# Kernel optimization log

Hardware: AMD Instinct MI355X
Metric: run time of the kernel (lower is better)

## Reference

```python
import jax, jax.numpy as jnp
import numpy as np

HEADS = 16

def rotate_half(x):
    x1, x2 = jnp.split(x, 2, axis=-1)
    return jnp.concatenate((-x2, x1), axis=-1)

def setup_inputs() -> dict:
    key = jax.random.key(0)
    k1, k2, k3, k4 = jax.random.split(key, 4)
    b, n, h = 2, 2048, 1024
    d = h // HEADS
    x = jax.random.normal(k1, (b, n, h), dtype=jnp.float32)
    rotary_emb = jax.random.normal(k2, (n, d), dtype=jnp.float32)
    w_qkv = jax.random.normal(k3, (h, 3 * h), dtype=jnp.float32) * (1.0 / np.sqrt(h))
    w_out = jax.random.normal(k4, (h, h), dtype=jnp.float32) * (1.0 / np.sqrt(h))
    return {"x": x, "rotary_emb": rotary_emb, "w_qkv": w_qkv, "w_out": w_out}

def reference(x, rotary_emb, w_qkv, w_out):
    b, n, hidden = x.shape
    d = hidden // HEADS
    # fused QKV projection: [b,n,3*hidden]
    qkv = jnp.einsum('bnh,hk->bnk', x, w_qkv)
    q, k, v = jnp.split(qkv, 3, axis=-1)
    # [b,n,hidden] -> [b,H,n,d]
    split_heads = lambda t: t.reshape(b, n, HEADS, d).transpose(0, 2, 1, 3)
    q, k, v = split_heads(q), split_heads(k), split_heads(v)
    # rotary: pos is [n,d], broadcast over batch/heads
    cos = jnp.cos(rotary_emb)[None, None]
    sin = jnp.sin(rotary_emb)[None, None]
    q = q * cos + rotate_half(q) * sin
    k = k * cos + rotate_half(k) * sin
    # SDPA (no mask, no dropout)
    scale = 1.0 / np.sqrt(d).astype(np.float32)
    scores = jnp.einsum('bhqd,bhkd->bhqk', q, k) * scale
    attn = jax.nn.softmax(scores, axis=-1)
    out = jnp.einsum('bhqk,bhkd->bhqd', attn, v)
    out = out.transpose(0, 2, 1, 3).reshape(b, n, hidden)
    return jnp.einsum('bnh,hk->bnk', out, w_out)
```

## Files before the change

### kernel.cpp

```cpp
#include <hip/hip_runtime.h>
#include <math.h>

#define HEADS 16
#define DH    64
#define SEQ   2048
#define HID   1024
#define NROW  4096

typedef __attribute__((ext_vector_type(8))) short bf16x8;
typedef __attribute__((ext_vector_type(4))) short bf16x4;
typedef __attribute__((ext_vector_type(4))) float f32x4;

#define AS1 __attribute__((address_space(1)))
#define AS3 __attribute__((address_space(3)))

#define QSCALE 0.18033688011112042f

__device__ __forceinline__ unsigned short f2bf(float x) {
    unsigned int u = __builtin_bit_cast(unsigned int, x);
    u = (u + 0x7FFFu + ((u >> 16) & 1u)) >> 16;
    return (unsigned short)u;
}

__device__ __forceinline__ void gload_lds16(const unsigned short* g, unsigned short* l) {
    __builtin_amdgcn_global_load_lds((AS1 void*)g, (AS3 void*)l, 16, 0, 0);
}

__device__ void wtrans_body(const float* __restrict__ wsrc, unsigned short* __restrict__ wt,
                            int K, int N, int bx, int by, float (*T)[65])
{
    const int tid = threadIdx.x;
    const int k0 = by * 64, n0 = bx * 64;
    #pragma unroll
    for (int rnd = 0; rnd < 4; ++rnd) {
        int row = (tid >> 4) + rnd * 16;
        int c = (tid & 15) * 4;
        float4 v = *(const float4*)&wsrc[(size_t)(k0 + row) * N + n0 + c];
        T[row][c] = v.x; T[row][c+1] = v.y; T[row][c+2] = v.z; T[row][c+3] = v.w;
    }
    __syncthreads();
    const int sr = tid >> 3, sc = (tid & 7) << 3;
    #pragma unroll
    for (int half = 0; half < 2; ++half) {
        int n = sr + half * 32;
        union { unsigned short u[8]; bf16x8 v; } pk;
        #pragma unroll
        for (int j = 0; j < 8; ++j) pk.u[j] = f2bf(T[sc + j][n]);
        *(bf16x8*)&wt[(size_t)(n0 + n) * K + k0 + sc] = pk.v;
    }
}

__global__ __launch_bounds__(256) void prep(const float* __restrict__ x,
                                            const float* __restrict__ rot,
                                            const float* __restrict__ w_qkv,
                                            const float* __restrict__ w_out,
                                            unsigned short* __restrict__ xb,
                                            float2* __restrict__ ctab,
                                            unsigned short* __restrict__ wqkvT,
                                            unsigned short* __restrict__ woutT)
{
    __shared__ float T[64][65];
    const int bid = blockIdx.x;
    if (bid < 2048) {
        size_t i = ((size_t)bid * 256 + threadIdx.x) * 8;
        float4 a = *(const float4*)&x[i];
        float4 b = *(const float4*)&x[i + 4];
        union { unsigned short u[8]; bf16x8 v; } pk;
        pk.u[0] = f2bf(a.x); pk.u[1] = f2bf(a.y); pk.u[2] = f2bf(a.z); pk.u[3] = f2bf(a.w);
        pk.u[4] = f2bf(b.x); pk.u[5] = f2bf(b.y); pk.u[6] = f2bf(b.z); pk.u[7] = f2bf(b.w);
        *(bf16x8*)&xb[i] = pk.v;
    } else if (bid < 2560) {
        int i = (bid - 2048) * 256 + threadIdx.x;
        float r = rot[i];
        float s, c;
        __sincosf(r, &s, &c);
        ctab[i] = make_float2(c, s);
    } else if (bid < 3328) {
        int idx = bid - 2560;
        wtrans_body(w_qkv, wqkvT, 1024, 3072, idx % 48, idx / 48, T);
    } else {
        int idx = bid - 3328;
        wtrans_body(w_out, woutT, 1024, 1024, idx % 16, idx / 16, T);
    }
}

__global__ __launch_bounds__(256) void gemm_qkv(const unsigned short* __restrict__ A,
                                                const unsigned short* __restrict__ Bt,
                                                const float2* __restrict__ ctab,
                                                unsigned short* __restrict__ qb,
                                                unsigned short* __restrict__ kb,
                                                unsigned short* __restrict__ vt)
{
    __shared__ __align__(16) unsigned short As[128 * 32];
    __shared__ __align__(16) unsigned short Bs[128 * 32];
    const int tid = threadIdx.x;
    const int w = tid >> 6, lane = tid & 63;
    const int quad = lane >> 4, lm = lane & 15;
    const int wr = (w >> 1) * 64, wc = (w & 1) * 64;
    const int bm = blockIdx.y * 128, bn = blockIdx.x * 128;
    const int m0 = tid >> 2;
    const int sk = (tid & 3) << 3;

    f32x4 acc[4][4];
    #pragma unroll
    for (int i = 0; i < 4; ++i)
        #pragma unroll
        for (int j = 0; j < 4; ++j) acc[i][j] = (f32x4){0.f, 0.f, 0.f, 0.f};

    for (int k0 = 0; k0 < 1024; k0 += 32) {
        __syncthreads();
        gload_lds16(&A [(size_t)(bm + m0     ) * 1024 + k0 + sk], As + (size_t)w * 512);
        gload_lds16(&A [(size_t)(bm + m0 + 64) * 1024 + k0 + sk], As + 2048 + (size_t)w * 512);
        gload_lds16(&Bt[(size_t)(bn + m0     ) * 1024 + k0 + sk], Bs + (size_t)w * 512);
        gload_lds16(&Bt[(size_t)(bn + m0 + 64) * 1024 + k0 + sk], Bs + 2048 + (size_t)w * 512);
        __syncthreads();
        bf16x8 af[4], bfr[4];
        #pragma unroll
        for (int mt = 0; mt < 4; ++mt) af[mt] = *(const bf16x8*)&As[(wr + mt * 16 + lm) * 32 + quad * 8];
        #pragma unroll
        for (int nt = 0; nt < 4; ++nt) bfr[nt] = *(const bf16x8*)&Bs[(wc + nt * 16 + lm) * 32 + quad * 8];
        #pragma unroll
        for (int mt = 0; mt < 4; ++mt)
            #pragma unroll
            for (int nt = 0; nt < 4; ++nt)
                acc[mt][nt] = __builtin_amdgcn_mfma_f32_16x16x32_bf16(af[mt], bfr[nt], acc[mt][nt], 0, 0, 0);
    }

    const int colbase = bn + wc;
    const int region = colbase >> 10;
    const int h = (colbase >> 6) & 15;

    if (region == 2) {
        #pragma unroll
        for (int mt = 0; mt < 4; ++mt) {
            int rowb = bm + wr + mt * 16 + quad * 4;
            int b = rowb >> 11, seq = rowb & (SEQ - 1);
            int t = seq >> 5, ks = seq & 31;
            #pragma unroll
            for (int nt = 0; nt < 4; ++nt) {
                int d = nt * 16 + lm;
                int ksw = (((ks >> 2) ^ (lm & 7)) << 2);
                ushort4 pk;
                pk.x = f2bf(acc[mt][nt][0]); pk.y = f2bf(acc[mt][nt][1]);
                pk.z = f2bf(acc[mt][nt][2]); pk.w = f2bf(acc[mt][nt][3]);
                *(ushort4*)&vt[(((size_t)(b * HEADS + h) * 64 + t) * 64 + d) * 32 + ksw] = pk;
            }
        }
    } else {
        const float qs = (region == 0) ? QSCALE : 1.0f;
        unsigned short* dst = (region == 0) ? qb : kb;
        #pragma unroll
        for (int mt = 0; mt < 4; ++mt) {
            #pragma unroll
            for (int nt = 0; nt < 2; ++nt) {
                int d = nt * 16 + lm;
                #pragma unroll
                for (int r = 0; r < 4; ++r) {
                    int row = bm + wr + mt * 16 + quad * 4 + r;
                    int b = row >> 11, seq = row & (SEQ - 1);
                    float2 cs0 = ctab[seq * DH + d];
                    float2 cs1 = ctab[seq * DH + d + 32];
                    float x0 = acc[mt][nt][r];
                    float x1 = acc[mt][nt + 2][r];
                    size_t ob = ((size_t)(b * HEADS + h) * SEQ + seq) * DH;
                    dst[ob + d]      = f2bf((x0 * cs0.x - x1 * cs0.y) * qs);
                    dst[ob + d + 32] = f2bf((x1 * cs1.x + x0 * cs1.y) * qs);
                }
            }
        }
    }
}

__global__ __launch_bounds__(256, 4) void attn13(const unsigned short* __restrict__ qb,
                                                 const unsigned short* __restrict__ kb,
                                                 const unsigned short* __restrict__ vt,
                                                 unsigned short* __restrict__ attnb)
{
    __shared__ __align__(16) char smem[32768];
    unsigned short* Ks = (unsigned short*)smem;
    unsigned short* Vs = (unsigned short*)(smem + 16384);

    const int tid = threadIdx.x;
    const int w = tid >> 6, lane = tid & 63, quad = lane >> 4, lm = lane & 15;
    const int qg = w >> 1, kg = w & 1;

    const int L = blockIdx.x + blockIdx.y * 32;
    const int bh = (L & 7) + 8 * ((L >> 3) & 3);
    const int q0 = (L >> 5) * 64;

    const int b = bh >> 4, h = bh & 15;
    const size_t hb = (size_t)bh * SEQ * DH;

    bf16x8 qf[2][2];
    #pragma unroll
    for (int qt = 0; qt < 2; ++qt)
        #pragma unroll
        for (int c = 0; c < 2; ++c)
            qf[qt][c] = *(const bf16x8*)&qb[hb + (size_t)(q0 + qg * 32 + qt * 16 + lm) * DH + c * 32 + quad * 8];

    const int r0 = (w * 16) + (lane >> 3);
    const int p0 = lane & 7;
    const int gk0 = r0 * 64 + (p0 ^ (r0 & 7)) * 8;
    const int r1 = r0 + 8;
    const int gk1 = r1 * 64 + (p0 ^ (r1 & 7)) * 8;
    const unsigned short* kgp = kb + hb;
    const unsigned short* vgp = vt + hb;
    const int gv0 = w * 1024 + lane * 8;
    const int gv1 = gv0 + 512;
    unsigned short* kdst0 = Ks + w * 1024;
    unsigned short* kdst1 = Ks + w * 1024 + 512;
    unsigned short* vdst0 = Vs + w * 1024;
    unsigned short* vdst1 = Vs + w * 1024 + 512;

    int kfo[2];
    #pragma unroll
    for (int c = 0; c < 2; ++c)
        kfo[c] = (kg * 32 + lm) * 64 + (((c * 4 + quad) ^ (lm & 7)) * 8);
    const int vrow = kg * 2048 + lm * 32;

    float rs[2] = {0.f, 0.f};
    f32x4 o[2][4];
    #pragma unroll
    for (int qt = 0; qt < 2; ++qt)
        #pragma unroll
        for (int dt = 0; dt < 4; ++dt) o[qt][dt] = (f32x4){0.f, 0.f, 0.f, 0.f};

    gload_lds16(kgp + gk0, kdst0);
    gload_lds16(kgp + gk1, kdst1);
    gload_lds16(vgp + gv0, vdst0);
    gload_lds16(vgp + gv1, vdst1);

    #pragma unroll 2
    for (int it = 0; it < 32; ++it) {
        const int buf = it & 1;
        __syncthreads();
        {
            const size_t nb = (size_t)((it + 1) & 31) * 4096;
            const int bo = (buf ^ 1) * 4096;
            gload_lds16(kgp + nb + gk0, kdst0 + bo);
            gload_lds16(kgp + nb + gk1, kdst1 + bo);
            gload_lds16(vgp + nb + gv0, vdst0 + bo);
            gload_lds16(vgp + nb + gv1, vdst1 + bo);
        }
        const unsigned short* Kb = Ks + buf * 4096;
        const unsigned short* Vb = Vs + buf * 4096;

        #pragma unroll
        for (int kt = 0; kt < 2; ++kt) {
            bf16x8 k0 = *(const bf16x8*)&Kb[kfo[0] + kt * 1024];
            bf16x8 k1 = *(const bf16x8*)&Kb[kfo[1] + kt * 1024];
            bf16x4 vb[4];
            #pragma unroll
            for (int dt = 0; dt < 4; ++dt)
                vb[dt] = *(const bf16x4*)&Vb[vrow + dt * 512 + (((kt * 4 + quad) ^ (lm & 7)) << 2)];
            f32x4 s[2];
            #pragma unroll
            for (int qt = 0; qt < 2; ++qt) {
                f32x4 z = (f32x4){0.f, 0.f, 0.f, 0.f};
                z = __builtin_amdgcn_mfma_f32_16x16x32_bf16(k0, qf[qt][0], z, 0, 0, 0);
                s[qt] = __builtin_amdgcn_mfma_f32_16x16x32_bf16(k1, qf[qt][1], z, 0, 0, 0);
            }
            #pragma unroll
            for (int qt = 0; qt < 2; ++qt) {
                unsigned int u[4];
                #pragma unroll
                for (int r = 0; r < 4; ++r) {
                    float p = __builtin_amdgcn_exp2f(s[qt][r]);
                    rs[qt] += p;
                    u[r] = __builtin_bit_cast(unsigned int, p);
                }
                union { unsigned int w2[2]; bf16x4 v; } pk;
                pk.w2[0] = __builtin_amdgcn_perm(u[1], u[0], 0x07060302);
                pk.w2[1] = __builtin_amdgcn_perm(u[3], u[2], 0x07060302);
                #pragma unroll
                for (int dt = 0; dt < 4; ++dt)
                    o[qt][dt] = __builtin_amdgcn_mfma_f32_16x16x16bf16_1k(pk.v, vb[dt], o[qt][dt], 0, 0, 0);
            }
        }
    }

    #pragma unroll
    for (int off = 16; off < 64; off <<= 1)
        #pragma unroll
        for (int qt = 0; qt < 2; ++qt) rs[qt] += __shfl_xor(rs[qt], off, 64);

    __syncthreads();
    float* oBuf = (float*)smem;
    float* lRed = (float*)(smem + 17408);
    if (kg == 1) {
        #pragma unroll
        for (int qt = 0; qt < 2; ++qt)
            #pragma unroll
            for (int dt = 0; dt < 4; ++dt)
                #pragma unroll
                for (int r = 0; r < 4; ++r)
                    oBuf[(qg * 32 + qt * 16 + quad * 4 + r) * 68 + dt * 16 + lm] = o[qt][dt][r];
        if (quad == 0) {
            #pragma unroll
            for (int qt = 0; qt < 2; ++qt) lRed[qg * 32 + qt * 16 + lm] = rs[qt];
        }
    }
    __syncthreads();
    if (kg == 0) {
        #pragma unroll
        for (int qt = 0; qt < 2; ++qt) {
            rs[qt] += lRed[qg * 32 + qt * 16 + lm];
            #pragma unroll
            for (int dt = 0; dt < 4; ++dt)
                #pragma unroll
                for (int r = 0; r < 4; ++r)
                    o[qt][dt][r] += oBuf[(qg * 32 + qt * 16 + quad * 4 + r) * 68 + dt * 16 + lm];
        }
        #pragma unroll
        for (int qt = 0; qt < 2; ++qt)
            #pragma unroll
            for (int r = 0; r < 4; ++r) {
                float inv = 1.0f / __shfl(rs[qt], quad * 4 + r, 64);
                int row = b * SEQ + q0 + qg * 32 + qt * 16 + quad * 4 + r;
                #pragma unroll
                for (int dt = 0; dt < 4; ++dt)
                    attnb[(size_t)row * HID + h * DH + dt * 16 + lm] = f2bf(o[qt][dt][r] * inv);
            }
    }
}

__global__ __launch_bounds__(256) void gemm_out(const unsigned short* __restrict__ A,
                                                const unsigned short* __restrict__ Bt,
                                                float* __restrict__ C)
{
    __shared__ __align__(16) unsigned short As[64 * 32];
    __shared__ __align__(16) unsigned short Bs[128 * 32];
    const int tid = threadIdx.x;
    const int w = tid >> 6, lane = tid & 63;
    const int quad = lane >> 4, lm = lane & 15;
    const int wr = (w >> 1) * 32, wc = (w & 1) * 64;
    const int bm = blockIdx.y * 64, bn = blockIdx.x * 128;
    const int m0 = tid >> 2;
    const int sk = (tid & 3) << 3;

    f32x4 acc[2][4];
    #pragma unroll
    for (int i = 0; i < 2; ++i)
        #pragma unroll
        for (int j = 0; j < 4; ++j) acc[i][j] = (f32x4){0.f, 0.f, 0.f, 0.f};

    for (int k0 = 0; k0 < 1024; k0 += 32) {
        __syncthreads();
        gload_lds16(&A [(size_t)(bm + m0     ) * 1024 + k0 + sk], As + (size_t)w * 512);
        gload_lds16(&Bt[(size_t)(bn + m0     ) * 1024 + k0 + sk], Bs + (size_t)w * 512);
        gload_lds16(&Bt[(size_t)(bn + m0 + 64) * 1024 + k0 + sk], Bs + 2048 + (size_t)w * 512);
        __syncthreads();
        bf16x8 af[2], bfr[4];
        #pragma unroll
        for (int mt = 0; mt < 2; ++mt) af[mt] = *(const bf16x8*)&As[(wr + mt * 16 + lm) * 32 + quad * 8];
        #pragma unroll
        for (int nt = 0; nt < 4; ++nt) bfr[nt] = *(const bf16x8*)&Bs[(wc + nt * 16 + lm) * 32 + quad * 8];
        #pragma unroll
        for (int mt = 0; mt < 2; ++mt)
            #pragma unroll
            for (int nt = 0; nt < 4; ++nt)
                acc[mt][nt] = __builtin_amdgcn_mfma_f32_16x16x32_bf16(af[mt], bfr[nt], acc[mt][nt], 0, 0, 0);
    }

    #pragma unroll
    for (int mt = 0; mt < 2; ++mt)
        #pragma unroll
        for (int nt = 0; nt < 4; ++nt) {
            int col = bn + wc + nt * 16 + lm;
            #pragma unroll
            for (int r = 0; r < 4; ++r) {
                int row = bm + wr + mt * 16 + quad * 4 + r;
                C[(size_t)row * 1024 + col] = acc[mt][nt][r];
            }
        }
}

extern "C" void kernel_launch(void* const* d_in, const int* in_sizes, int n_in,
                              void* d_out, int out_size, void* d_ws, size_t ws_size,
                              hipStream_t stream) {
    const float* x     = (const float*)d_in[0];
    const float* rot   = (const float*)d_in[1];
    const float* w_qkv = (const float*)d_in[2];
    const float* w_out = (const float*)d_in[3];
    float* out = (float*)d_out;

    char* ws = (char*)d_ws;
    unsigned short* xb    = (unsigned short*)(ws);
    unsigned short* qb    = (unsigned short*)(ws + (size_t)( 8u << 20));
    unsigned short* kb    = (unsigned short*)(ws + (size_t)(16u << 20));
    unsigned short* vt    = (unsigned short*)(ws + (size_t)(24u << 20));
    unsigned short* attnb = (unsigned short*)(ws + (size_t)(32u << 20));
    unsigned short* wqkvT = (unsigned short*)(ws + (size_t)(40u << 20));
    unsigned short* woutT = (unsigned short*)(ws + (size_t)(46u << 20));
    float2*         ctab  = (float2*)        (ws + (size_t)(48u << 20));

    prep<<<3584, 256, 0, stream>>>(x, rot, w_qkv, w_out, xb, ctab, wqkvT, woutT);

    gemm_qkv<<<dim3(24, 32), 256, 0, stream>>>(xb, wqkvT, ctab, qb, kb, vt);

    attn13<<<dim3(32, 32), 256, 0, stream>>>(qb, kb, vt, attnb);

    gemm_out<<<dim3(8, 64), 256, 0, stream>>>(attnb, woutT, out);
}
```

Baseline: 197.5 us.

## Double-buffer LDS tiles and XOR-swizzle K chunks in both GEMMs

Both the QKV and output projection GEMMs now use two LDS buffers. The next K tile is issued asynchronously into the spare buffer while MFMAs run on the current one, which removes one barrier per iteration and overlaps global loads with compute. The 16-byte K chunks are also XOR-swizzled by row on store and on fragment read to cut LDS bank conflicts. This doubles LDS use per block, which may lower occupancy, and it adds one harmless wrap-around prefetch on the last iteration.

```diff
diff --git a/kernel.cpp b/kernel.cpp
--- a/kernel.cpp
+++ b/kernel.cpp
@@ -91,15 +91,16 @@
                                                 unsigned short* __restrict__ kb,
                                                 unsigned short* __restrict__ vt)
 {
-    __shared__ __align__(16) unsigned short As[128 * 32];
-    __shared__ __align__(16) unsigned short Bs[128 * 32];
+    __shared__ __align__(16) unsigned short As[2][128 * 32];
+    __shared__ __align__(16) unsigned short Bs[2][128 * 32];
     const int tid = threadIdx.x;
     const int w = tid >> 6, lane = tid & 63;
     const int quad = lane >> 4, lm = lane & 15;
     const int wr = (w >> 1) * 64, wc = (w & 1) * 64;
     const int bm = blockIdx.y * 128, bn = blockIdx.x * 128;
     const int m0 = tid >> 2;
-    const int sk = (tid & 3) << 3;
+    const int sk = (((tid & 3) ^ ((m0 >> 1) & 3)) << 3);
+    const int kx = ((quad ^ ((lm >> 1) & 3)) << 3);
 
     f32x4 acc[4][4];
     #pragma unroll
@@ -107,18 +108,27 @@
         #pragma unroll
         for (int j = 0; j < 4; ++j) acc[i][j] = (f32x4){0.f, 0.f, 0.f, 0.f};
 
-    for (int k0 = 0; k0 < 1024; k0 += 32) {
+    gload_lds16(&A [(size_t)(bm + m0     ) * 1024 + sk], &As[0][w * 512]);
+    gload_lds16(&A [(size_t)(bm + m0 + 64) * 1024 + sk], &As[0][2048 + w * 512]);
+    gload_lds16(&Bt[(size_t)(bn + m0     ) * 1024 + sk], &Bs[0][w * 512]);
+    gload_lds16(&Bt[(size_t)(bn + m0 + 64) * 1024 + sk], &Bs[0][2048 + w * 512]);
+
+    #pragma unroll 2
+    for (int it = 0; it < 32; ++it) {
+        const int buf = it & 1;
         __syncthreads();
-        gload_lds16(&A [(size_t)(bm + m0     ) * 1024 + k0 + sk], As + (size_t)w * 512);
-        gload_lds16(&A [(size_t)(bm + m0 + 64) * 1024 + k0 + sk], As + 2048 + (size_t)w * 512);
-        gload_lds16(&Bt[(size_t)(bn + m0     ) * 1024 + k0 + sk], Bs + (size_t)w * 512);
-        gload_lds16(&Bt[(size_t)(bn + m0 + 64) * 1024 + k0 + sk], Bs + 2048 + (size_t)w * 512);
-        __syncthreads();
+        {
+            const int nk = ((it + 1) & 31) * 32;
+            gload_lds16(&A [(size_t)(bm + m0     ) * 1024 + nk + sk], &As[buf ^ 1][w * 512]);
+            gload_lds16(&A [(size_t)(bm + m0 + 64) * 1024 + nk + sk], &As[buf ^ 1][2048 + w * 512]);
+            gload_lds16(&Bt[(size_t)(bn + m0     ) * 1024 + nk + sk], &Bs[buf ^ 1][w * 512]);
+            gload_lds16(&Bt[(size_t)(bn + m0 + 64) * 1024 + nk + sk], &Bs[buf ^ 1][2048 + w * 512]);
+        }
         bf16x8 af[4], bfr[4];
         #pragma unroll
-        for (int mt = 0; mt < 4; ++mt) af[mt] = *(const bf16x8*)&As[(wr + mt * 16 + lm) * 32 + quad * 8];
-        #pragma unroll
-        for (int nt = 0; nt < 4; ++nt) bfr[nt] = *(const bf16x8*)&Bs[(wc + nt * 16 + lm) * 32 + quad * 8];
+        for (int mt = 0; mt < 4; ++mt) af[mt] = *(const bf16x8*)&As[buf][(wr + mt * 16 + lm) * 32 + kx];
+        #pragma unroll
+        for (int nt = 0; nt < 4; ++nt) bfr[nt] = *(const bf16x8*)&Bs[buf][(wc + nt * 16 + lm) * 32 + kx];
         #pragma unroll
         for (int mt = 0; mt < 4; ++mt)
             #pragma unroll
@@ -328,15 +338,16 @@
                                                 const unsigned short* __restrict__ Bt,
                                                 float* __restrict__ C)
 {
-    __shared__ __align__(16) unsigned short As[64 * 32];
-    __shared__ __align__(16) unsigned short Bs[128 * 32];
+    __shared__ __align__(16) unsigned short As[2][64 * 32];
+    __shared__ __align__(16) unsigned short Bs[2][128 * 32];
     const int tid = threadIdx.x;
     const int w = tid >> 6, lane = tid & 63;
     const int quad = lane >> 4, lm = lane & 15;
     const int wr = (w >> 1) * 32, wc = (w & 1) * 64;
     const int bm = blockIdx.y * 64, bn = blockIdx.x * 128;
     const int m0 = tid >> 2;
-    const int sk = (tid & 3) << 3;
+    const int sk = (((tid & 3) ^ ((m0 >> 1) & 3)) << 3);
+    const int kx = ((quad ^ ((lm >> 1) & 3)) << 3);
 
     f32x4 acc[2][4];
     #pragma unroll
@@ -344,17 +355,25 @@
         #pragma unroll
         for (int j = 0; j < 4; ++j) acc[i][j] = (f32x4){0.f, 0.f, 0.f, 0.f};
 
-    for (int k0 = 0; k0 < 1024; k0 += 32) {
+    gload_lds16(&A [(size_t)(bm + m0     ) * 1024 + sk], &As[0][w * 512]);
+    gload_lds16(&Bt[(size_t)(bn + m0     ) * 1024 + sk], &Bs[0][w * 512]);
+    gload_lds16(&Bt[(size_t)(bn + m0 + 64) * 1024 + sk], &Bs[0][2048 + w * 512]);
+
+    #pragma unroll 2
+    for (int it = 0; it < 32; ++it) {
+        const int buf = it & 1;
         __syncthreads();
-        gload_lds16(&A [(size_t)(bm + m0     ) * 1024 + k0 + sk], As + (size_t)w * 512);
-        gload_lds16(&Bt[(size_t)(bn + m0     ) * 1024 + k0 + sk], Bs + (size_t)w * 512);
-        gload_lds16(&Bt[(size_t)(bn + m0 + 64) * 1024 + k0 + sk], Bs + 2048 + (size_t)w * 512);
-        __syncthreads();
+        {
+            const int nk = ((it + 1) & 31) * 32;
+            gload_lds16(&A [(size_t)(bm + m0     ) * 1024 + nk + sk], &As[buf ^ 1][w * 512]);
+            gload_lds16(&Bt[(size_t)(bn + m0     ) * 1024 + nk + sk], &Bs[buf ^ 1][w * 512]);
+            gload_lds16(&Bt[(size_t)(bn + m0 + 64) * 1024 + nk + sk], &Bs[buf ^ 1][2048 + w * 512]);
+        }
         bf16x8 af[2], bfr[4];
         #pragma unroll
-        for (int mt = 0; mt < 2; ++mt) af[mt] = *(const bf16x8*)&As[(wr + mt * 16 + lm) * 32 + quad * 8];
-        #pragma unroll
-        for (int nt = 0; nt < 4; ++nt) bfr[nt] = *(const bf16x8*)&Bs[(wc + nt * 16 + lm) * 32 + quad * 8];
+        for (int mt = 0; mt < 2; ++mt) af[mt] = *(const bf16x8*)&As[buf][(wr + mt * 16 + lm) * 32 + kx];
+        #pragma unroll
+        for (int nt = 0; nt < 4; ++nt) bfr[nt] = *(const bf16x8*)&Bs[buf][(wc + nt * 16 + lm) * 32 + kx];
         #pragma unroll
         for (int mt = 0; mt < 2; ++mt)
             #pragma unroll
```

New measurement: 202.0 us. 2.3% more time.
